# Optimization experiments

Measured on AMD Instinct MI355X. Metric: run time of the kernel, lower is better.

Reference implementation:

```python
import jax, jax.numpy as jnp
import numpy as np

N_NODES = 100000
N_EDGES = 1600000
IN_DIM, HID, OUT_DIM = 128, 128, 64


def _glorot(key, fan_in, fan_out):
    s = float(np.sqrt(6.0 / (fan_in + fan_out)))
    return jax.random.uniform(key, (fan_in, fan_out), jnp.float32, -s, s)


def setup_inputs() -> dict:
    key = jax.random.key(0)
    ks = jax.random.split(key, 6)
    x = jax.random.normal(ks[0], (N_NODES, IN_DIM), jnp.float32)
    edge_index = jax.random.randint(ks[1], (2, N_EDGES), 0, N_NODES, jnp.int32)
    return {
        "x": x,
        "edge_index": edge_index,
        "W0": _glorot(ks[2], IN_DIM, HID), "b0": jnp.zeros((HID,), jnp.float32),
        "W1": _glorot(ks[3], HID, HID),    "b1": jnp.zeros((HID,), jnp.float32),
        "W2": _glorot(ks[4], HID, OUT_DIM), "b2": jnp.zeros((OUT_DIM,), jnp.float32),
    }


def _gcn_conv(x, src, dst, norm, W, b):
    # x' = D^{-1/2} (A+I) D^{-1/2} X W + b  (PyG GCNConv, add_self_loops=True)
    h = x @ W                       # [N, F_out]
    msg = h[src] * norm[:, None]    # [E+N, F_out] gathered, normalized messages
    out = jax.ops.segment_sum(msg, dst, num_segments=x.shape[0])
    return out + b


def reference(x, edge_index, W0, b0, W1, b1, W2, b2):
    n = x.shape[0]
    loop = jnp.arange(n, dtype=edge_index.dtype)
    src = jnp.concatenate([edge_index[0], loop])  # self-loops appended
    dst = jnp.concatenate([edge_index[1], loop])
    deg = jax.ops.segment_sum(jnp.ones_like(src, jnp.float32), dst, num_segments=n)
    dis = jnp.where(deg > 0, jax.lax.rsqrt(jnp.maximum(deg, 1e-12)), 0.0)
    norm = dis[src] * dis[dst]      # symmetric GCN normalization per edge

    h = jax.nn.relu(_gcn_conv(x, src, dst, norm, W0, b0))
    h = jax.nn.relu(_gcn_conv(h, src, dst, norm, W1, b1))
    h = jax.nn.relu(_gcn_conv(h, src, dst, norm, W2, b2))
    return jax.nn.log_softmax(h, axis=1)
```

## Files before the change

kernel.cpp:

```cpp
#include <hip/hip_runtime.h>

#define NN 100000
#define NE 1600000
#define NBK 782
#define NBLK 256
#define CHUNK ((NE + NBLK - 1) / NBLK)

typedef __bf16 bf16x8 __attribute__((ext_vector_type(8)));
typedef float f32x2 __attribute__((ext_vector_type(2)));
typedef float f32x4 __attribute__((ext_vector_type(4)));

#define ACC8_FP8(vv)                                                                  \
  {                                                                                   \
    f32x2 p;                                                                          \
    p = __builtin_amdgcn_cvt_pk_f32_fp8((vv).x, 0); acc[0] += p[0]; acc[1] += p[1];   \
    p = __builtin_amdgcn_cvt_pk_f32_fp8((vv).x, 1); acc[2] += p[0]; acc[3] += p[1];   \
    p = __builtin_amdgcn_cvt_pk_f32_fp8((vv).y, 0); acc[4] += p[0]; acc[5] += p[1];   \
    p = __builtin_amdgcn_cvt_pk_f32_fp8((vv).y, 1); acc[6] += p[0]; acc[7] += p[1];   \
  }


__global__ __launch_bounds__(256) void kW_prep(const float* __restrict__ W0, const float* __restrict__ W1,
                                               const float* __restrict__ W2, __bf16* __restrict__ Wt) {
  int i = blockIdx.x * 256 + threadIdx.x;
  if (i < 16384) {
    int k = i >> 7, n = i & 127;
    Wt[n * 128 + k] = (__bf16)W0[i];
  } else if (i < 32768) {
    int j = i - 16384;
    int k = j >> 7, n = j & 127;
    Wt[16384 + n * 128 + k] = (__bf16)W1[j];
  } else if (i < 40960) {
    int j = i - 32768;
    int k = j >> 6, n = j & 63;
    Wt[32768 + n * 128 + k] = (__bf16)W2[j];
  }
}


__global__ __launch_bounds__(256) void k1_hist(const int* __restrict__ dst, int* __restrict__ bhist) {
  __shared__ int h[NBK];
  int tid = threadIdx.x, b = blockIdx.x;
  for (int i = tid; i < NBK; i += 256) h[i] = 0;
  __syncthreads();
  int base = b * CHUNK, end = min(base + CHUNK, NE);
  for (int e = base + tid; e < end; e += 256) atomicAdd(&h[dst[e] >> 7], 1);
  __syncthreads();
  for (int i = tid; i < NBK; i += 256) bhist[i * NBLK + b] = h[i];
}

__global__ __launch_bounds__(256) void kA2(const int* __restrict__ bhist, int* __restrict__ btot) {
  int w = threadIdx.x >> 6, lane = threadIdx.x & 63;
  int bin = blockIdx.x * 4 + w;
  if (bin >= NBK) return;
  int4 v = *(const int4*)(bhist + bin * NBLK + lane * 4);
  int s = v.x + v.y + v.z + v.w;
#pragma unroll
  for (int off = 32; off > 0; off >>= 1) s += __shfl_xor(s, off);
  if (lane == 0) btot[bin] = s;
}

__global__ __launch_bounds__(1024) void kB_bscan(const int* __restrict__ btot, int* __restrict__ bptr) {
  __shared__ int s[1024];
  int tid = threadIdx.x;
  int v = (tid < NBK) ? btot[tid] : 0;
  s[tid] = v;
  __syncthreads();
  for (int off = 1; off < 1024; off <<= 1) {
    int t = (tid >= off) ? s[tid - off] : 0;
    __syncthreads();
    s[tid] += t;
    __syncthreads();
  }
  if (tid < NBK) bptr[tid + 1] = s[tid];
  if (tid == 0) bptr[0] = 0;
}

__global__ __launch_bounds__(256) void kC2(const int* __restrict__ bhist, const int* __restrict__ bptr,
                                           int* __restrict__ blockbase) {
  int w = threadIdx.x >> 6, lane = threadIdx.x & 63;
  int bin = blockIdx.x * 4 + w;
  if (bin >= NBK) return;
  int4 v = *(const int4*)(bhist + bin * NBLK + lane * 4);
  int ls = v.x + v.y + v.z + v.w;
  int incl = ls;
#pragma unroll
  for (int off = 1; off < 64; off <<= 1) {
    int t = __shfl_up(incl, off);
    if (lane >= off) incl += t;
  }
  int base = bptr[bin] + incl - ls;
  int4 o;
  o.x = base;
  o.y = base + v.x;
  o.z = base + v.x + v.y;
  o.w = base + v.x + v.y + v.z;
  *(int4*)(blockbase + bin * NBLK + lane * 4) = o;
}

__global__ __launch_bounds__(256) void k3_scatter(const int* __restrict__ src, const int* __restrict__ dst,
                                                  const int* __restrict__ blockbase, int* __restrict__ bucketed) {
  __shared__ int cur[NBK];
  int tid = threadIdx.x, b = blockIdx.x;
  for (int i = tid; i < NBK; i += 256) cur[i] = blockbase[i * NBLK + b];
  __syncthreads();
  int base = b * CHUNK, end = min(base + CHUNK, NE);
  for (int e = base + tid; e < end; e += 256) {
    int d = dst[e];
    int pos = atomicAdd(&cur[d >> 7], 1);
    bucketed[pos] = (src[e] << 7) | (d & 127);
  }
}

__global__ __launch_bounds__(256) void k_degfill(const int* __restrict__ bucketed, const int* __restrict__ bptr,
                                                 int* __restrict__ row_ptr, float* __restrict__ dis,
                                                 int* __restrict__ csr_src) {
  __shared__ int deg[128];
  __shared__ int sc[128];
  __shared__ int cur[128];
  int b = blockIdx.x, tid = threadIdx.x;
  int nb0 = b << 7;
  if (tid < 128) deg[tid] = 0;
  __syncthreads();
  int beg = bptr[b], end = bptr[b + 1];
  for (int e = beg + tid; e < end; e += 256) atomicAdd(&deg[bucketed[e] & 127], 1);
  __syncthreads();
  if (tid < 128) sc[tid] = deg[tid];
  __syncthreads();
  for (int off = 1; off < 128; off <<= 1) {
    int t = (tid >= off && tid < 128) ? sc[tid - off] : 0;
    __syncthreads();
    if (tid < 128) sc[tid] += t;
    __syncthreads();
  }
  if (tid < 128) {
    cur[tid] = beg + sc[tid] - deg[tid];
    if (nb0 + tid < NN) {
      row_ptr[nb0 + tid + 1] = beg + sc[tid];
      dis[nb0 + tid] = rsqrtf((float)(deg[tid] + 1));
      if (b == 0 && tid == 0) row_ptr[0] = 0;
    }
  }
  __syncthreads();
  for (int e = beg + tid; e < end; e += 256) {
    int pk = bucketed[e];
    int pos = atomicAdd(&cur[pk & 127], 1);
    csr_src[pos] = pk >> 7;
  }
}


template <int BN, int MODE, bool OUT8>
__global__ __launch_bounds__(256) void k_gemm(const void* __restrict__ Av, const __bf16* __restrict__ Wt,
                                              const float* __restrict__ bias, const float* __restrict__ dis,
                                              void* __restrict__ outv) {
  constexpr int LDK = 136;
  constexpr int NT = BN / 32;
  constexpr int ROWB = BN * (OUT8 ? 1 : 2);
  __shared__ __bf16 lB[BN * LDK];

  const int tid = threadIdx.x;
  const int rowBase = blockIdx.x * 128;
  const int lane = tid & 63;
  const int wid = tid >> 6;
  const int wm = (wid & 1) * 64;
  const int wn = (wid >> 1) * (BN / 2);
  const int lm = lane & 15;
  const int kg = lane >> 4;

  if (blockIdx.x == 0 && tid < ROWB / 16) {
    ((uint4*)((char*)outv + (size_t)NN * ROWB))[tid] = make_uint4(0, 0, 0, 0);
  }

  for (int c = tid; c < 16 * BN; c += 256) {
    int n = c >> 4;
    int koff = (c & 15) * 8;
    bf16x8 w = *(const bf16x8*)(Wt + n * 128 + koff);
    *(bf16x8*)&lB[n * LDK + koff] = w;
  }
  __syncthreads();

  f32x4 acc[4][NT] = {};
  const bool full = (rowBase + 128 <= NN);

#pragma unroll 2
  for (int ks = 0; ks < 128; ks += 32) {
    int k0 = ks + kg * 8;
    bf16x8 af[4];
    if constexpr (MODE == 0) {
      const float* A = (const float*)Av;
#pragma unroll
      for (int tm = 0; tm < 4; ++tm) {
        int gr = rowBase + wm + tm * 16 + lm;
        f32x4 a0 = {}, a1 = {};
        if (full || gr < NN) {
          a0 = *(const f32x4*)(A + (size_t)gr * 128 + k0);
          a1 = *(const f32x4*)(A + (size_t)gr * 128 + k0 + 4);
        }
        af[tm] = bf16x8{(__bf16)a0[0], (__bf16)a0[1], (__bf16)a0[2], (__bf16)a0[3],
                        (__bf16)a1[0], (__bf16)a1[1], (__bf16)a1[2], (__bf16)a1[3]};
      }
    } else {
      const __bf16* A = (const __bf16*)Av;
      f32x4 b0 = *(const f32x4*)(bias + k0);
      f32x4 b1 = *(const f32x4*)(bias + k0 + 4);
#pragma unroll
      for (int tm = 0; tm < 4; ++tm) {
        int gr = rowBase + wm + tm * 16 + lm;
        bf16x8 v = {};
        if (full || gr < NN) v = *(const bf16x8*)(A + (size_t)gr * 128 + k0);
        af[tm] = bf16x8{(__bf16)fmaxf((float)v[0] + b0[0], 0.f), (__bf16)fmaxf((float)v[1] + b0[1], 0.f),
                        (__bf16)fmaxf((float)v[2] + b0[2], 0.f), (__bf16)fmaxf((float)v[3] + b0[3], 0.f),
                        (__bf16)fmaxf((float)v[4] + b1[0], 0.f), (__bf16)fmaxf((float)v[5] + b1[1], 0.f),
                        (__bf16)fmaxf((float)v[6] + b1[2], 0.f), (__bf16)fmaxf((float)v[7] + b1[3], 0.f)};
      }
    }
    bf16x8 bfr[NT];
#pragma unroll
    for (int tn = 0; tn < NT; ++tn)
      bfr[tn] = *(const bf16x8*)&lB[(wn + tn * 16 + lm) * LDK + k0];
#pragma unroll
    for (int tm = 0; tm < 4; ++tm)
#pragma unroll
      for (int tn = 0; tn < NT; ++tn)
        acc[tm][tn] = __builtin_amdgcn_mfma_f32_16x16x32_bf16(af[tm], bfr[tn], acc[tm][tn], 0, 0, 0);
  }

#pragma unroll
  for (int tm = 0; tm < 4; ++tm) {
    int r0 = rowBase + wm + tm * 16 + kg * 4;
#pragma unroll
    for (int tn = 0; tn < NT; ++tn) {
      int c0 = wn + tn * 16 + lm;
#pragma unroll
      for (int r = 0; r < 4; ++r) {
        int gr = r0 + r;
        if (full || gr < NN) {
          float val = acc[tm][tn][r] * dis[gr];
          if constexpr (OUT8) {
            unsigned char* o8 = (unsigned char*)outv;
            unsigned pk = __builtin_amdgcn_cvt_pk_fp8_f32(val, val, 0, 0);
            o8[(size_t)gr * BN + c0] = (unsigned char)(pk & 0xffu);
          } else {
            __bf16* ob = (__bf16*)outv;
            ob[(size_t)gr * BN + c0] = (__bf16)val;
          }
        }
      }
    }
  }
}


__global__ __launch_bounds__(256) void k_agg128(const unsigned char* __restrict__ tmp8, const int* __restrict__ row_ptr,
                                                const int* __restrict__ csr_src, const float* __restrict__ dis,
                                                __bf16* __restrict__ agg) {
  int wid = (blockIdx.x * 256 + threadIdx.x) >> 6;
  int lane = threadIdx.x & 63;
  if (wid >= NN) return;
  int grp = lane >> 4;
  int fl = lane & 15;

  int beg = row_ptr[wid];
  int end = row_ptr[wid + 1];

  float acc[8] = {0.f, 0.f, 0.f, 0.f, 0.f, 0.f, 0.f, 0.f};
  if (grp == 0) {
    uint2 sv = *(const uint2*)(tmp8 + (size_t)wid * 128 + fl * 8);
    ACC8_FP8(sv);
  }

  for (int base = beg; base < end; base += 64) {
    int cnt = min(64, end - base);
    int sidx = (base + lane < end) ? csr_src[base + lane] : NN;
    int i = 0;
    while (i < cnt) {
      int rem = cnt - i;
      if (rem > 16) {
        uint2 v[8];
#pragma unroll
        for (int u = 0; u < 8; ++u) {
          int s = __shfl(sidx, (i + u * 4 + grp) & 63);
          v[u] = *(const uint2*)(tmp8 + (size_t)s * 128 + fl * 8);
        }
#pragma unroll
        for (int u = 0; u < 8; ++u) ACC8_FP8(v[u]);
        i += 32;
      } else {
        uint2 v[4];
#pragma unroll
        for (int u = 0; u < 4; ++u) {
          int s = __shfl(sidx, (i + u * 4 + grp) & 63);
          v[u] = *(const uint2*)(tmp8 + (size_t)s * 128 + fl * 8);
        }
#pragma unroll
        for (int u = 0; u < 4; ++u) ACC8_FP8(v[u]);
        i += 16;
      }
    }
  }

#pragma unroll
  for (int t = 0; t < 8; ++t) acc[t] += __shfl_xor(acc[t], 16);
#pragma unroll
  for (int t = 0; t < 8; ++t) acc[t] += __shfl_xor(acc[t], 32);

  if (grp == 0) {
    float d = dis[wid];
    bf16x8 o;
#pragma unroll
    for (int t = 0; t < 8; ++t) o[t] = (__bf16)(acc[t] * d);
    *(bf16x8*)&agg[(size_t)wid * 128 + fl * 8] = o;
  }
}


__global__ __launch_bounds__(256) void k_agg64_final(const __bf16* __restrict__ tmp, const int* __restrict__ row_ptr,
                                                     const int* __restrict__ csr_src, const float* __restrict__ dis,
                                                     const float* __restrict__ b2, float* __restrict__ out) {
  __shared__ float xch[4][8][66];
  int tid = threadIdx.x;
  int wv = tid >> 6;
  int wid = (blockIdx.x * 256 + tid) >> 6;
  int lane = tid & 63;
  int grp = lane >> 3;
  int fl = lane & 7;

  int beg = row_ptr[wid];
  int end = row_ptr[wid + 1];

  float acc[8];
  {
    bf16x8 sv = {};
    if (grp == 0) sv = *(const bf16x8*)&tmp[(size_t)wid * 64 + fl * 8];
#pragma unroll
    for (int t = 0; t < 8; ++t) acc[t] = (grp == 0) ? (float)sv[t] : 0.f;
  }

  for (int base = beg; base < end; base += 64) {
    int cnt = min(64, end - base);
    int sidx = (base + lane < end) ? csr_src[base + lane] : NN;
    int i = 0;
    while (i < cnt) {
      int rem = cnt - i;
      if (rem > 32) {
        bf16x8 v[8];
#pragma unroll
        for (int u = 0; u < 8; ++u) {
          int s = __shfl(sidx, (i + u * 8 + grp) & 63);
          v[u] = *(const bf16x8*)&tmp[(size_t)s * 64 + fl * 8];
        }
#pragma unroll
        for (int u = 0; u < 8; ++u)
#pragma unroll
          for (int t = 0; t < 8; ++t) acc[t] += (float)v[u][t];
        i += 64;
      } else if (rem > 16) {
        bf16x8 v[4];
#pragma unroll
        for (int u = 0; u < 4; ++u) {
          int s = __shfl(sidx, (i + u * 8 + grp) & 63);
          v[u] = *(const bf16x8*)&tmp[(size_t)s * 64 + fl * 8];
        }
#pragma unroll
        for (int u = 0; u < 4; ++u)
#pragma unroll
          for (int t = 0; t < 8; ++t) acc[t] += (float)v[u][t];
        i += 32;
      } else if (rem > 8) {
        bf16x8 v[2];
#pragma unroll
        for (int u = 0; u < 2; ++u) {
          int s = __shfl(sidx, (i + u * 8 + grp) & 63);
          v[u] = *(const bf16x8*)&tmp[(size_t)s * 64 + fl * 8];
        }
#pragma unroll
        for (int u = 0; u < 2; ++u)
#pragma unroll
          for (int t = 0; t < 8; ++t) acc[t] += (float)v[u][t];
        i += 16;
      } else {
        int s = __shfl(sidx, (i + grp) & 63);
        bf16x8 v = *(const bf16x8*)&tmp[(size_t)s * 64 + fl * 8];
#pragma unroll
        for (int t = 0; t < 8; ++t) acc[t] += (float)v[t];
        i += 8;
      }
    }
  }

  *(f32x2*)&xch[wv][grp][fl * 8 + 0] = f32x2{acc[0], acc[1]};
  *(f32x2*)&xch[wv][grp][fl * 8 + 2] = f32x2{acc[2], acc[3]};
  *(f32x2*)&xch[wv][grp][fl * 8 + 4] = f32x2{acc[4], acc[5]};
  *(f32x2*)&xch[wv][grp][fl * 8 + 6] = f32x2{acc[6], acc[7]};
  __syncthreads();
  float av = 0.f;
#pragma unroll
  for (int g = 0; g < 8; ++g) av += xch[wv][g][lane];

  float v = fmaxf(av * dis[wid] + b2[lane], 0.f);
  float lm = v;
#pragma unroll
  for (int off = 32; off > 0; off >>= 1) lm = fmaxf(lm, __shfl_xor(lm, off));
  float e = __expf(v - lm);
  float le = e;
#pragma unroll
  for (int off = 32; off > 0; off >>= 1) le += __shfl_xor(le, off);
  out[(size_t)wid * 64 + lane] = v - lm - __logf(le);
}


extern "C" void kernel_launch(void* const* d_in, const int* in_sizes, int n_in,
                              void* d_out, int out_size, void* d_ws, size_t ws_size,
                              hipStream_t stream) {
  const float* x  = (const float*)d_in[0];
  const int*   ei = (const int*)d_in[1];
  const float* W0 = (const float*)d_in[2];
  const float* b0 = (const float*)d_in[3];
  const float* W1 = (const float*)d_in[4];
  const float* b1 = (const float*)d_in[5];
  const float* W2 = (const float*)d_in[6];
  const float* b2 = (const float*)d_in[7];
  const int* esrc = ei;
  const int* edst = ei + NE;

  char* p = (char*)d_ws;
  auto alloc = [&](size_t bytes) {
    char* q = p;
    p += (bytes + 255) & ~(size_t)255;
    return q;
  };
  float*  dis     = (float*)alloc((size_t)NN * 4);
  int*    row_ptr = (int*)alloc((size_t)(NN + 1) * 4);
  int*    btot    = (int*)alloc(NBK * 4);
  int*    bptr    = (int*)alloc((NBK + 1) * 4);
  __bf16* Wt      = (__bf16*)alloc(40960 * 2);
  int*    csr_src = (int*)alloc((size_t)NE * 4);
  char*   tmp     = (char*)alloc((size_t)(NN + 1) * 128 * 2);
  unsigned char* tmp8 = (unsigned char*)tmp;
  __bf16* tmp16   = (__bf16*)tmp;
  int*    bucketed  = (int*)tmp;
  int*    bhist     = csr_src;
  int*    blockbase = csr_src + NBLK * NBK;

  kW_prep<<<160, 256, 0, stream>>>(W0, W1, W2, Wt);
  k1_hist<<<NBLK, 256, 0, stream>>>(edst, bhist);
  kA2<<<(NBK + 3) / 4, 256, 0, stream>>>(bhist, btot);
  kB_bscan<<<1, 1024, 0, stream>>>(btot, bptr);
  kC2<<<(NBK + 3) / 4, 256, 0, stream>>>(bhist, bptr, blockbase);
  k3_scatter<<<NBLK, 256, 0, stream>>>(esrc, edst, blockbase, bucketed);
  k_degfill<<<NBK, 256, 0, stream>>>(bucketed, bptr, row_ptr, dis, csr_src);

  int gblocks = (NN + 127) / 128;
  int ablocks = (NN * 64 + 255) / 256;

  k_gemm<128, 0, true><<<gblocks, 256, 0, stream>>>(x, Wt, nullptr, dis, tmp8);
  k_agg128<<<ablocks, 256, 0, stream>>>(tmp8, row_ptr, csr_src, dis, (__bf16*)d_out);

  k_gemm<128, 2, true><<<gblocks, 256, 0, stream>>>(d_out, Wt + 16384, b0, dis, tmp8);
  k_agg128<<<ablocks, 256, 0, stream>>>(tmp8, row_ptr, csr_src, dis, (__bf16*)d_out);

  k_gemm<64, 2, false><<<gblocks, 256, 0, stream>>>(d_out, Wt + 32768, b1, dis, tmp16);
  k_agg64_final<<<ablocks, 256, 0, stream>>>(tmp16, row_ptr, csr_src, dis, b2, (float*)d_out);
}
```

Baseline: 381.2 us.

## Widen agg128 gathers to 16 bytes, fuse weight prep, shuffle-based scans and softmax

The 128-wide aggregation now has each lane load 16 fp8 bytes instead of 8, so 8 edges are processed per wave step instead of 4, with finer tail handling. The final 64-wide aggregation replaces its shared-memory exchange and barrier with a cross-lane shuffle reduction and a per-lane 8-wide log-softmax. The weight-transpose kernel is merged into the histogram launch as extra blocks, and the block scan switches from a barrier-heavy shared-memory loop to wave shuffles. Together these aim to cut memory transactions, launches and synchronisation, at the cost of more accumulator registers and a dropped bounds check in agg128.

```diff
diff --git a/kernel.cpp b/kernel.cpp
--- a/kernel.cpp
+++ b/kernel.cpp
@@ -6,41 +6,47 @@
 #define NBLK 256
 #define CHUNK ((NE + NBLK - 1) / NBLK)
 
+typedef __bf16 bf16x4 __attribute__((ext_vector_type(4)));
 typedef __bf16 bf16x8 __attribute__((ext_vector_type(8)));
 typedef float f32x2 __attribute__((ext_vector_type(2)));
 typedef float f32x4 __attribute__((ext_vector_type(4)));
 
-#define ACC8_FP8(vv)                                                                  \
-  {                                                                                   \
-    f32x2 p;                                                                          \
-    p = __builtin_amdgcn_cvt_pk_f32_fp8((vv).x, 0); acc[0] += p[0]; acc[1] += p[1];   \
-    p = __builtin_amdgcn_cvt_pk_f32_fp8((vv).x, 1); acc[2] += p[0]; acc[3] += p[1];   \
-    p = __builtin_amdgcn_cvt_pk_f32_fp8((vv).y, 0); acc[4] += p[0]; acc[5] += p[1];   \
-    p = __builtin_amdgcn_cvt_pk_f32_fp8((vv).y, 1); acc[6] += p[0]; acc[7] += p[1];   \
-  }
-
-
-__global__ __launch_bounds__(256) void kW_prep(const float* __restrict__ W0, const float* __restrict__ W1,
+#define ACC16_FP8(vv)                                                                   \
+  {                                                                                     \
+    f32x2 p;                                                                            \
+    p = __builtin_amdgcn_cvt_pk_f32_fp8((vv).x, 0); acc[0] += p[0];  acc[1] += p[1];    \
+    p = __builtin_amdgcn_cvt_pk_f32_fp8((vv).x, 1); acc[2] += p[0];  acc[3] += p[1];    \
+    p = __builtin_amdgcn_cvt_pk_f32_fp8((vv).y, 0); acc[4] += p[0];  acc[5] += p[1];    \
+    p = __builtin_amdgcn_cvt_pk_f32_fp8((vv).y, 1); acc[6] += p[0];  acc[7] += p[1];    \
+    p = __builtin_amdgcn_cvt_pk_f32_fp8((vv).z, 0); acc[8] += p[0];  acc[9] += p[1];    \
+    p = __builtin_amdgcn_cvt_pk_f32_fp8((vv).z, 1); acc[10] += p[0]; acc[11] += p[1];   \
+    p = __builtin_amdgcn_cvt_pk_f32_fp8((vv).w, 0); acc[12] += p[0]; acc[13] += p[1];   \
+    p = __builtin_amdgcn_cvt_pk_f32_fp8((vv).w, 1); acc[14] += p[0]; acc[15] += p[1];   \
+  }
+
+
+__global__ __launch_bounds__(256) void k1_hist(const int* __restrict__ dst, int* __restrict__ bhist,
+                                               const float* __restrict__ W0, const float* __restrict__ W1,
                                                const float* __restrict__ W2, __bf16* __restrict__ Wt) {
-  int i = blockIdx.x * 256 + threadIdx.x;
-  if (i < 16384) {
-    int k = i >> 7, n = i & 127;
-    Wt[n * 128 + k] = (__bf16)W0[i];
-  } else if (i < 32768) {
-    int j = i - 16384;
-    int k = j >> 7, n = j & 127;
-    Wt[16384 + n * 128 + k] = (__bf16)W1[j];
-  } else if (i < 40960) {
-    int j = i - 32768;
-    int k = j >> 6, n = j & 63;
-    Wt[32768 + n * 128 + k] = (__bf16)W2[j];
-  }
-}
-
-
-__global__ __launch_bounds__(256) void k1_hist(const int* __restrict__ dst, int* __restrict__ bhist) {
+  int b = blockIdx.x;
+  if (b >= NBLK) {
+    int i = (b - NBLK) * 256 + threadIdx.x;
+    if (i < 16384) {
+      int k = i >> 7, n = i & 127;
+      Wt[n * 128 + k] = (__bf16)W0[i];
+    } else if (i < 32768) {
+      int j = i - 16384;
+      int k = j >> 7, n = j & 127;
+      Wt[16384 + n * 128 + k] = (__bf16)W1[j];
+    } else if (i < 40960) {
+      int j = i - 32768;
+      int k = j >> 6, n = j & 63;
+      Wt[32768 + n * 128 + k] = (__bf16)W2[j];
+    }
+    return;
+  }
   __shared__ int h[NBK];
-  int tid = threadIdx.x, b = blockIdx.x;
+  int tid = threadIdx.x;
   for (int i = tid; i < NBK; i += 256) h[i] = 0;
   __syncthreads();
   int base = b * CHUNK, end = min(base + CHUNK, NE);
@@ -61,18 +67,29 @@
 }
 
 __global__ __launch_bounds__(1024) void kB_bscan(const int* __restrict__ btot, int* __restrict__ bptr) {
-  __shared__ int s[1024];
-  int tid = threadIdx.x;
+  __shared__ int ws[16];
+  int tid = threadIdx.x, lane = tid & 63, w = tid >> 6;
   int v = (tid < NBK) ? btot[tid] : 0;
-  s[tid] = v;
-  __syncthreads();
-  for (int off = 1; off < 1024; off <<= 1) {
-    int t = (tid >= off) ? s[tid - off] : 0;
-    __syncthreads();
-    s[tid] += t;
-    __syncthreads();
-  }
-  if (tid < NBK) bptr[tid + 1] = s[tid];
+  int incl = v;
+#pragma unroll
+  for (int off = 1; off < 64; off <<= 1) {
+    int t = __shfl_up(incl, off);
+    if (lane >= off) incl += t;
+  }
+  if (lane == 63) ws[w] = incl;
+  __syncthreads();
+  if (tid < 16) {
+    int s = ws[tid];
+    int si = s;
+#pragma unroll
+    for (int off = 1; off < 16; off <<= 1) {
+      int t = __shfl_up(si, off);
+      if (lane >= off) si += t;
+    }
+    ws[tid] = si - s;
+  }
+  __syncthreads();
+  if (tid < NBK) bptr[tid + 1] = incl + ws[w];
   if (tid == 0) bptr[0] = 0;
 }
 
@@ -257,17 +274,16 @@
                                                 __bf16* __restrict__ agg) {
   int wid = (blockIdx.x * 256 + threadIdx.x) >> 6;
   int lane = threadIdx.x & 63;
-  if (wid >= NN) return;
-  int grp = lane >> 4;
-  int fl = lane & 15;
+  int grp = lane >> 3;
+  int fl = lane & 7;
 
   int beg = row_ptr[wid];
   int end = row_ptr[wid + 1];
 
-  float acc[8] = {0.f, 0.f, 0.f, 0.f, 0.f, 0.f, 0.f, 0.f};
+  float acc[16] = {};
   if (grp == 0) {
-    uint2 sv = *(const uint2*)(tmp8 + (size_t)wid * 128 + fl * 8);
-    ACC8_FP8(sv);
+    uint4 sv = *(const uint4*)(tmp8 + (size_t)wid * 128 + fl * 16);
+    ACC16_FP8(sv);
   }
 
   for (int base = beg; base < end; base += 64) {
@@ -276,41 +292,61 @@
     int i = 0;
     while (i < cnt) {
       int rem = cnt - i;
-      if (rem > 16) {
-        uint2 v[8];
+      if (rem > 32) {
+        uint4 v[8];
 #pragma unroll
         for (int u = 0; u < 8; ++u) {
-          int s = __shfl(sidx, (i + u * 4 + grp) & 63);
-          v[u] = *(const uint2*)(tmp8 + (size_t)s * 128 + fl * 8);
-        }
-#pragma unroll
-        for (int u = 0; u < 8; ++u) ACC8_FP8(v[u]);
+          int s = __shfl(sidx, (i + u * 8 + grp) & 63);
+          v[u] = *(const uint4*)(tmp8 + (size_t)s * 128 + fl * 16);
+        }
+#pragma unroll
+        for (int u = 0; u < 8; ++u) ACC16_FP8(v[u]);
+        i += 64;
+      } else if (rem > 16) {
+        uint4 v[4];
+#pragma unroll
+        for (int u = 0; u < 4; ++u) {
+          int s = __shfl(sidx, (i + u * 8 + grp) & 63);
+          v[u] = *(const uint4*)(tmp8 + (size_t)s * 128 + fl * 16);
+        }
+#pragma unroll
+        for (int u = 0; u < 4; ++u) ACC16_FP8(v[u]);
         i += 32;
+      } else if (rem > 8) {
+        uint4 v[2];
+#pragma unroll
+        for (int u = 0; u < 2; ++u) {
+          int s = __shfl(sidx, (i + u * 8 + grp) & 63);
+          v[u] = *(const uint4*)(tmp8 + (size_t)s * 128 + fl * 16);
+        }
+#pragma unroll
+        for (int u = 0; u < 2; ++u) ACC16_FP8(v[u]);
+        i += 16;
       } else {
-        uint2 v[4];
-#pragma unroll
-        for (int u = 0; u < 4; ++u) {
-          int s = __shfl(sidx, (i + u * 4 + grp) & 63);
-          v[u] = *(const uint2*)(tmp8 + (size_t)s * 128 + fl * 8);
-        }
-#pragma unroll
-        for (int u = 0; u < 4; ++u) ACC8_FP8(v[u]);
-        i += 16;
+        int s = __shfl(sidx, (i + grp) & 63);
+        uint4 v = *(const uint4*)(tmp8 + (size_t)s * 128 + fl * 16);
+        ACC16_FP8(v);
+        i += 8;
       }
     }
   }
 
 #pragma unroll
-  for (int t = 0; t < 8; ++t) acc[t] += __shfl_xor(acc[t], 16);
-#pragma unroll
-  for (int t = 0; t < 8; ++t) acc[t] += __shfl_xor(acc[t], 32);
+  for (int t = 0; t < 16; ++t) acc[t] += __shfl_xor(acc[t], 8);
+#pragma unroll
+  for (int t = 0; t < 16; ++t) acc[t] += __shfl_xor(acc[t], 16);
+#pragma unroll
+  for (int t = 0; t < 16; ++t) acc[t] += __shfl_xor(acc[t], 32);
 
   if (grp == 0) {
     float d = dis[wid];
-    bf16x8 o;
-#pragma unroll
-    for (int t = 0; t < 8; ++t) o[t] = (__bf16)(acc[t] * d);
-    *(bf16x8*)&agg[(size_t)wid * 128 + fl * 8] = o;
+    bf16x8 o0, o1;
+#pragma unroll
+    for (int t = 0; t < 8; ++t) o0[t] = (__bf16)(acc[t] * d);
+#pragma unroll
+    for (int t = 0; t < 8; ++t) o1[t] = (__bf16)(acc[8 + t] * d);
+    *(bf16x8*)&agg[(size_t)wid * 128 + fl * 16] = o0;
+    *(bf16x8*)&agg[(size_t)wid * 128 + fl * 16 + 8] = o1;
   }
 }
 
@@ -318,23 +354,19 @@
 __global__ __launch_bounds__(256) void k_agg64_final(const __bf16* __restrict__ tmp, const int* __restrict__ row_ptr,
                                                      const int* __restrict__ csr_src, const float* __restrict__ dis,
                                                      const float* __restrict__ b2, float* __restrict__ out) {
-  __shared__ float xch[4][8][66];
-  int tid = threadIdx.x;
-  int wv = tid >> 6;
-  int wid = (blockIdx.x * 256 + tid) >> 6;
-  int lane = tid & 63;
+  int wid = (blockIdx.x * 256 + threadIdx.x) >> 6;
+  int lane = threadIdx.x & 63;
   int grp = lane >> 3;
   int fl = lane & 7;
 
   int beg = row_ptr[wid];
   int end = row_ptr[wid + 1];
 
-  float acc[8];
-  {
-    bf16x8 sv = {};
-    if (grp == 0) sv = *(const bf16x8*)&tmp[(size_t)wid * 64 + fl * 8];
-#pragma unroll
-    for (int t = 0; t < 8; ++t) acc[t] = (grp == 0) ? (float)sv[t] : 0.f;
+  float acc[8] = {};
+  if (grp == 0) {
+    bf16x8 sv = *(const bf16x8*)&tmp[(size_t)wid * 64 + fl * 8];
+#pragma unroll
+    for (int t = 0; t < 8; ++t) acc[t] = (float)sv[t];
   }
 
   for (int base = beg; base < end; base += 64) {
@@ -389,24 +421,34 @@
     }
   }
 
-  *(f32x2*)&xch[wv][grp][fl * 8 + 0] = f32x2{acc[0], acc[1]};
-  *(f32x2*)&xch[wv][grp][fl * 8 + 2] = f32x2{acc[2], acc[3]};
-  *(f32x2*)&xch[wv][grp][fl * 8 + 4] = f32x2{acc[4], acc[5]};
-  *(f32x2*)&xch[wv][grp][fl * 8 + 6] = f32x2{acc[6], acc[7]};
-  __syncthreads();
-  float av = 0.f;
-#pragma unroll
-  for (int g = 0; g < 8; ++g) av += xch[wv][g][lane];
-
-  float v = fmaxf(av * dis[wid] + b2[lane], 0.f);
-  float lm = v;
-#pragma unroll
-  for (int off = 32; off > 0; off >>= 1) lm = fmaxf(lm, __shfl_xor(lm, off));
-  float e = __expf(v - lm);
-  float le = e;
-#pragma unroll
-  for (int off = 32; off > 0; off >>= 1) le += __shfl_xor(le, off);
-  out[(size_t)wid * 64 + lane] = v - lm - __logf(le);
+#pragma unroll
+  for (int t = 0; t < 8; ++t) acc[t] += __shfl_xor(acc[t], 8);
+#pragma unroll
+  for (int t = 0; t < 8; ++t) acc[t] += __shfl_xor(acc[t], 16);
+#pragma unroll
+  for (int t = 0; t < 8; ++t) acc[t] += __shfl_xor(acc[t], 32);
+
+  float d = dis[wid];
+  float v[8], lm = -1e30f;
+#pragma unroll
+  for (int t = 0; t < 8; ++t) {
+    v[t] = fmaxf(acc[t] * d + b2[fl * 8 + t], 0.f);
+    lm = fmaxf(lm, v[t]);
+  }
+#pragma unroll
+  for (int off = 4; off > 0; off >>= 1) lm = fmaxf(lm, __shfl_xor(lm, off));
+  float le = 0.f;
+#pragma unroll
+  for (int t = 0; t < 8; ++t) le += __expf(v[t] - lm);
+#pragma unroll
+  for (int off = 4; off > 0; off >>= 1) le += __shfl_xor(le, off);
+  float ls = lm + __logf(le);
+  if (grp == 0) {
+    f32x4 o0 = {v[0] - ls, v[1] - ls, v[2] - ls, v[3] - ls};
+    f32x4 o1 = {v[4] - ls, v[5] - ls, v[6] - ls, v[7] - ls};
+    *(f32x4*)&out[(size_t)wid * 64 + fl * 8] = o0;
+    *(f32x4*)&out[(size_t)wid * 64 + fl * 8 + 4] = o1;
+  }
 }
 
 
@@ -443,8 +485,7 @@
   int*    bhist     = csr_src;
   int*    blockbase = csr_src + NBLK * NBK;
 
-  kW_prep<<<160, 256, 0, stream>>>(W0, W1, W2, Wt);
-  k1_hist<<<NBLK, 256, 0, stream>>>(edst, bhist);
+  k1_hist<<<NBLK + 160, 256, 0, stream>>>(edst, bhist, W0, W1, W2, Wt);
   kA2<<<(NBK + 3) / 4, 256, 0, stream>>>(bhist, btot);
   kB_bscan<<<1, 1024, 0, stream>>>(btot, bptr);
   kC2<<<(NBK + 3) / 4, 256, 0, stream>>>(bhist, bptr, blockbase);
```

New measurement: 452.7 us. 1.19x slower.
